# Kernel optimization log

Hardware: AMD Instinct MI355X
Metric: run time of the kernel (lower is better)

The kernel has to match this reference:

```python
import jax, jax.numpy as jnp
import numpy as np

B, T, DM, H = 2, 2048, 2048, 16
D = DM // H  # 128
STD = 0.02


def setup_inputs() -> dict:
    key = jax.random.key(0)
    ks = jax.random.split(key, 8)
    inner = H * D
    x = jax.random.normal(ks[0], (B, T, DM), jnp.float32)
    state = jnp.zeros((B, H, D, D), jnp.float32)
    Wq = jax.random.normal(ks[1], (inner, DM), jnp.float32) * STD
    Wk = jax.random.normal(ks[2], (inner, DM), jnp.float32) * STD
    Wv = jax.random.normal(ks[3], (inner, DM), jnp.float32) * STD
    Wa = jax.random.normal(ks[4], (inner, DM), jnp.float32) * STD
    ba = jnp.zeros((inner,), jnp.float32)
    Wb = jax.random.normal(ks[5], (H, DM), jnp.float32) * STD
    bb = jnp.zeros((H,), jnp.float32)
    Wg = jax.random.normal(ks[6], (inner, DM), jnp.float32) * STD
    bg = jnp.zeros((inner,), jnp.float32)
    Wo = jax.random.normal(ks[7], (DM, inner), jnp.float32) * STD
    return {"x": x, "state": state, "Wq": Wq, "Wk": Wk, "Wv": Wv,
            "Wa": Wa, "ba": ba, "Wb": Wb, "bb": bb, "Wg": Wg, "bg": bg, "Wo": Wo}


def _l2norm(t):
    # matches torch F.normalize(p=2, dim=-1, eps=1e-12)
    n = jnp.sqrt(jnp.sum(t * t, axis=-1, keepdims=True))
    return t / jnp.maximum(n, 1e-12)


def reference(x, state, Wq, Wk, Wv, Wa, ba, Wb, bb, Wg, bg, Wo):
    b, t, _ = x.shape
    q = _l2norm((x @ Wq.T).reshape(b, t, H, D))
    k = _l2norm((x @ Wk.T).reshape(b, t, H, D))
    v = (x @ Wv.T).reshape(b, t, H, D)
    alpha = jax.nn.sigmoid(x @ Wa.T + ba).reshape(b, t, H, D)
    beta = jax.nn.sigmoid(x @ Wb.T + bb)  # (B,T,H)

    def step(S, inp):
        q_t, k_t, v_t, a_t, b_t = inp  # (B,H,D) x4, (B,H)
        Sk = jnp.einsum('bhij,bhj->bhi', S, k_t)
        delta = v_t - Sk
        S = a_t[..., None] * S + (b_t[..., None] * delta)[..., None] * k_t[:, :, None, :]
        out_t = jnp.einsum('bhij,bhj->bhi', S, q_t)
        return S, out_t

    xs = tuple(jnp.moveaxis(a, 1, 0) for a in (q, k, v, alpha, beta))
    _, outs = jax.lax.scan(step, state, xs)  # outs: (T,B,H,D)
    out = jnp.moveaxis(outs, 0, 1)  # (B,T,H,D)
    g = jax.nn.sigmoid(x @ Wg.T + bg).reshape(b, t, H, D)
    out = (out * g).reshape(b, t, H * D) @ Wo.T
    return out
```

## Files before the change

kernel.cpp:

```cpp
#include <hip/hip_runtime.h>
#include <hip/hip_bf16.h>

typedef short short8 __attribute__((ext_vector_type(8)));
typedef float f32x4 __attribute__((ext_vector_type(4)));

#define DEV __device__ __forceinline__
#define AS1 __attribute__((address_space(1)))
#define AS3 __attribute__((address_space(3)))

DEV void async_load16(const void* g, void* l) {
    __builtin_amdgcn_global_load_lds((const AS1 unsigned int*)g, (AS3 unsigned int*)l, 16, 0, 0);
}

template <int CTRL>
DEV float dpp_add16(float v) {
    int t = __builtin_amdgcn_update_dpp(0, __float_as_int(v), CTRL, 0xf, 0xf, true);
    return v + __int_as_float(t);
}
DEV float row_sum16(float v) {
    v = dpp_add16<0x128>(v);
    v = dpp_add16<0x124>(v);
    v = dpp_add16<0x122>(v);
    v = dpp_add16<0x121>(v);
    return v;
}

__global__ __launch_bounds__(256) void cast_bf16_kernel(const float* __restrict__ in,
                                                        __hip_bfloat16* __restrict__ out, int n) {
    int i = (blockIdx.x * 256 + threadIdx.x) * 4;
    if (i < n) {
        float4 v = *(const float4*)&in[i];
        out[i + 0] = __float2bfloat16(v.x);
        out[i + 1] = __float2bfloat16(v.y);
        out[i + 2] = __float2bfloat16(v.z);
        out[i + 3] = __float2bfloat16(v.w);
    }
}

__global__ __launch_bounds__(256) void cast6_kernel(const float* __restrict__ s0, const float* __restrict__ s1,
                                                    const float* __restrict__ s2, const float* __restrict__ s3,
                                                    const float* __restrict__ s4, const float* __restrict__ s5,
                                                    __hip_bfloat16* __restrict__ dst) {
    const int sec = blockIdx.x >> 12;
    const int loc = blockIdx.x & 4095;
    const float* s = sec == 0 ? s0 : sec == 1 ? s1 : sec == 2 ? s2 : sec == 3 ? s3 : sec == 4 ? s4 : s5;
    const int i = (loc * 256 + threadIdx.x) * 4;
    float4 v = *(const float4*)&s[i];
    __hip_bfloat16* o = dst + (size_t)sec * 4194304 + i;
    o[0] = __float2bfloat16(v.x);
    o[1] = __float2bfloat16(v.y);
    o[2] = __float2bfloat16(v.z);
    o[3] = __float2bfloat16(v.w);
}

template <int EPI>
__global__ __launch_bounds__(512, 2) void gemm256_fused(
        const short* __restrict__ A, const short* __restrict__ Bm,
        float* __restrict__ C, const float* __restrict__ bias1,
        const float* __restrict__ bias2, int M, int N, int K) {
    __shared__ short lds_s[65536];

    const int tid  = threadIdx.x;
    const int lane = tid & 63;
    const int w    = tid >> 6;
    const int wave_m = w >> 2;
    const int wave_n = w & 3;
    const int fr  = lane & 15;
    const int fk2 = (lane >> 4) * 16;
    const int er  = (lane >> 4) * 4;
    const int ec  = lane & 15;

    const int nbx = M >> 8;
    const int wg  = blockIdx.x;
    const int nwg = gridDim.x;
    const int cpx = nwg >> 3;
    const int swz = (wg & 7) * cpx + (wg >> 3);
    const int m0 = (swz & (nbx - 1)) * 256;
    const int n0 = (swz / nbx) * 256;

    const int Kb = K * 2;

    f32x4 acc[8][4] = {};

#define AREG(d, kh) (((d) * 2 + (kh)) << 14)
#define BREG(d, kh) (65536 + (((d) * 2 + (kh)) << 14))

    const int sr0 = w * 32 + (lane >> 2);
    const int sr1 = sr0 + 16;
    const int kbl = (lane & 3) * 16;
    auto STAGE = [&](const short* mat, int rc0, int tkoff, int region) {
        const char* g0 = (const char*)mat + (size_t)(rc0 + sr0) * Kb + tkoff + (kbl ^ (((sr0 >> 1) & 3) << 4));
        const char* g1 = (const char*)mat + (size_t)(rc0 + sr1) * Kb + tkoff + (kbl ^ (((sr1 >> 1) & 3) << 4));
        async_load16(g0, &lds_s[(region + w * 2048) >> 1]);
        async_load16(g1, &lds_s[(region + w * 2048 + 1024) >> 1]);
    };
    auto RDA = [&](int region, int i) -> short8 {
        const int ra = wave_m * 128 + i * 16 + fr;
        return *(const short8*)&lds_s[(region + ra * 64 + (fk2 ^ (((ra >> 1) & 3) << 4))) >> 1];
    };
    auto RDB = [&](int region, int j) -> short8 {
        const int cl = wave_n * 64 + j * 16 + fr;
        return *(const short8*)&lds_s[(region + cl * 64 + (fk2 ^ (((cl >> 1) & 3) << 4))) >> 1];
    };

    STAGE(A,  m0, 0,   AREG(0, 0));  STAGE(A,  m0, 64,  AREG(0, 1));
    STAGE(Bm, n0, 0,   BREG(0, 0));  STAGE(Bm, n0, 64,  BREG(0, 1));
    STAGE(A,  m0, 128, AREG(1, 0));  STAGE(A,  m0, 192, AREG(1, 1));
    STAGE(Bm, n0, 128, BREG(1, 0));  STAGE(Bm, n0, 192, BREG(1, 1));
    asm volatile("s_waitcnt vmcnt(0)" ::: "memory");
    __builtin_amdgcn_s_barrier();
    __builtin_amdgcn_sched_barrier(0);

    short8 af[8], b0, b1;
    const int NT = K >> 6;

#define MFMA8(JA, JB)                                                            \
    __builtin_amdgcn_s_setprio(1);                                               \
    _Pragma("unroll") for (int i = 0; i < 8; i++)                                \
        acc[i][JA] = __builtin_amdgcn_mfma_f32_16x16x32_bf16(af[i], b0, acc[i][JA], 0, 0, 0); \
    _Pragma("unroll") for (int i = 0; i < 8; i++)                                \
        acc[i][JB] = __builtin_amdgcn_mfma_f32_16x16x32_bf16(af[i], b1, acc[i][JB], 0, 0, 0); \
    __builtin_amdgcn_s_setprio(0);

#define ENDPH()                                                                  \
    __builtin_amdgcn_s_barrier();                                                \
    __builtin_amdgcn_sched_barrier(0);

#define KTILE(D, T)                                                              \
    {                                                                            \
        _Pragma("unroll") for (int i = 0; i < 8; i++) af[i] = RDA(AREG(D, 0), i);\
        b0 = RDB(BREG(D, 0), 0); b1 = RDB(BREG(D, 0), 1);                        \
        STAGE(Bm, n0, ((T) + 1) * 128 + 64, BREG(D ^ 1, 1));                     \
        MFMA8(0, 1)                                                              \
        ENDPH()                                                                  \
        b0 = RDB(BREG(D, 0), 2); b1 = RDB(BREG(D, 0), 3);                        \
        STAGE(A, m0, ((T) + 2) * 128, AREG(D, 0));                               \
        MFMA8(2, 3)                                                              \
        ENDPH()                                                                  \
        _Pragma("unroll") for (int i = 0; i < 8; i++) af[i] = RDA(AREG(D, 1), i);\
        b0 = RDB(BREG(D, 1), 0); b1 = RDB(BREG(D, 1), 1);                        \
        STAGE(Bm, n0, ((T) + 2) * 128, BREG(D, 0));                              \
        MFMA8(0, 1)                                                              \
        ENDPH()                                                                  \
        b0 = RDB(BREG(D, 1), 2); b1 = RDB(BREG(D, 1), 3);                        \
        STAGE(A, m0, ((T) + 2) * 128 + 64, AREG(D, 1));                          \
        MFMA8(2, 3)                                                              \
        asm volatile("s_waitcnt vmcnt(6)" ::: "memory");                         \
        ENDPH()                                                                  \
    }

    for (int T = 0; T < NT; T += 2) {
        KTILE(0, T)
        KTILE(1, T + 1)
    }
#undef KTILE
#undef ENDPH
#undef MFMA8

    if constexpr (EPI == 2) {
        const bool isqk = (n0 < 4096);
        if (isqk) {
            __syncthreads();
            float* lsum = (float*)lds_s;
#pragma unroll
            for (int i = 0; i < 8; i++) {
                float p[4];
#pragma unroll
                for (int r = 0; r < 4; r++) {
                    float s = acc[i][0][r] * acc[i][0][r] + acc[i][1][r] * acc[i][1][r]
                            + acc[i][2][r] * acc[i][2][r] + acc[i][3][r] * acc[i][3][r];
                    p[r] = row_sum16(s);
                }
                if (ec == 0) {
                    const int R = wave_m * 128 + i * 16 + er;
                    lsum[wave_n * 256 + R + 0] = p[0];
                    lsum[wave_n * 256 + R + 1] = p[1];
                    lsum[wave_n * 256 + R + 2] = p[2];
                    lsum[wave_n * 256 + R + 3] = p[3];
                }
            }
            __syncthreads();
            const int h0 = (wave_n & 2);
#pragma unroll
            for (int i = 0; i < 8; i++)
#pragma unroll
                for (int r = 0; r < 4; r++) {
                    const int R = wave_m * 128 + i * 16 + er + r;
                    const float tot = lsum[h0 * 256 + R] + lsum[(h0 + 1) * 256 + R];
                    const float inv = 1.f / fmaxf(sqrtf(tot), 1e-12f);
#pragma unroll
                    for (int j = 0; j < 4; j++) acc[i][j][r] *= inv;
                }
        }
    }

    bool sig = false;
    const float* bp = nullptr;
    if constexpr (EPI == 2) {
        sig = (n0 >= 6144);
        if (sig) bp = (n0 >= 8192) ? (bias2 + (n0 - 8192)) : (bias1 + (n0 - 6144));
    }

#pragma unroll
    for (int i = 0; i < 8; i++) {
        const int gr = m0 + wave_m * 128 + i * 16 + er;
#pragma unroll
        for (int j = 0; j < 4; j++) {
            const int gc = n0 + wave_n * 64 + j * 16 + ec;
            float bia = 0.f;
            if constexpr (EPI == 2) { if (sig) bia = bp[wave_n * 64 + j * 16 + ec]; }
#pragma unroll
            for (int r = 0; r < 4; r++) {
                float v = acc[i][j][r];
                if constexpr (EPI == 2) { if (sig) v = 1.f / (1.f + __expf(-(v + bia))); }
                C[(size_t)(gr + r) * N + gc] = v;
            }
        }
    }
    asm volatile("s_waitcnt vmcnt(0)" ::: "memory");
}

__global__ __launch_bounds__(256) void beta_kernel(const float* __restrict__ x,
                                                   const float* __restrict__ Wb,
                                                   const float* __restrict__ bb,
                                                   float* __restrict__ beta) {
    __shared__ float xs[16 * 132];
    const int tid = threadIdx.x;
    const float* xr = &x[(size_t)blockIdx.x * 2048];
#pragma unroll
    for (int i = tid; i < 512; i += 256) {
        float4 v = ((const float4*)xr)[i];
        const int j = i * 4;
        *(float4*)&xs[(j >> 7) * 132 + (j & 127)] = v;
    }
    __syncthreads();
    const int n = tid >> 4, ks = tid & 15;
    const float* wv = &Wb[(size_t)n * 2048 + ks * 128];
    const float* xx = &xs[ks * 132];
    float s = 0.f;
#pragma unroll 8
    for (int j = 0; j < 128; j++) s += xx[j] * wv[j];
    s += __shfl_xor(s, 1); s += __shfl_xor(s, 2);
    s += __shfl_xor(s, 4); s += __shfl_xor(s, 8);
    if (ks == 0) beta[(size_t)blockIdx.x * 16 + n] = 1.f / (1.f + __expf(-(s + bb[n])));
}

__global__ __launch_bounds__(256)
__attribute__((amdgpu_waves_per_eu(1, 1)))
void recurrence_kernel(
        const float* __restrict__ S0, const float* __restrict__ qall,
        const float* __restrict__ bet, __hip_bfloat16* __restrict__ o) {
    __shared__ __hip_bfloat16 lout[4][64][4];

    const int bh  = blockIdx.x & 31;
    const int rb8 = blockIdx.x >> 5;
    const int b = bh >> 4, h = bh & 15;
    const int lane = threadIdx.x & 63;
    const int wave = threadIdx.x >> 6;
    const int r = lane >> 4;
    const int c = lane & 15;
    const int i0 = rb8 * 16 + wave * 4;
    const int i = i0 + r;

    f32x4 S40, S41;
    {
        const float* s0 = &S0[((size_t)(bh * 128 + i)) * 128 + c * 8];
        S40 = *(const f32x4*)s0;
        S41 = *(const f32x4*)(s0 + 4);
    }

    const unsigned SB = 10240 * 4;
    const float* rowb = qall + (size_t)(b * 2048) * 10240 + h * 128;
    const float* qbase = rowb;
    const float* kbase = rowb + 2048;
    const float* vbase = rowb + 4096;
    const float* abase = rowb + 6144;
    const float* gbase = rowb + 8192;
    const float* bbase = bet + (size_t)(b * 2048) * 16 + h;
    char* ob = (char*)(o + ((size_t)(b * 2048) * 16 + h) * 128 + i0);

    unsigned voff_kq = (unsigned)(c * 32);
    unsigned voff_i  = (unsigned)(i * 4);
    unsigned voff_b  = 0;

    f32x4 kA0, kA1, qA0, qA1; float vA, aA, gA, bA;
    f32x4 kB0, kB1, qB0, qB1; float vB, aB, gB, bB;
    f32x4 kC0, kC1, qC0, qC1; float vC, aC, gC, bC;
    f32x4 kD0, kD1, qD0, qD1; float vD, aD, gD, bD;

#define ISSUE(SET)                                                              \
    asm volatile("global_load_dwordx4 %0, %2, %3\n\t"                           \
                 "global_load_dwordx4 %1, %2, %3 offset:16"                     \
                 : "=v"(k##SET##0), "=v"(k##SET##1)                             \
                 : "v"(voff_kq), "s"(kbase));                                   \
    asm volatile("global_load_dwordx4 %0, %2, %3\n\t"                           \
                 "global_load_dwordx4 %1, %2, %3 offset:16"                     \
                 : "=v"(q##SET##0), "=v"(q##SET##1)                             \
                 : "v"(voff_kq), "s"(qbase));                                   \
    asm volatile("global_load_dword %0, %1, %2"                                 \
                 : "=v"(v##SET) : "v"(voff_i), "s"(vbase));                     \
    asm volatile("global_load_dword %0, %1, %2"                                 \
                 : "=v"(a##SET) : "v"(voff_i), "s"(abase));                     \
    asm volatile("global_load_dword %0, %1, %2"                                 \
                 : "=v"(g##SET) : "v"(voff_i), "s"(gbase));                     \
    asm volatile("global_load_dword %0, %1, %2"                                 \
                 : "=v"(b##SET) : "v"(voff_b), "s"(bbase));

#define ADV() { voff_kq += SB; voff_i += SB; voff_b += 64; }

    ISSUE(A); ADV();
    ISSUE(B); ADV();
    ISSUE(C); ADV();
    ISSUE(D); ADV();

#define BODY(SLOT, SET)                                                   \
    {                                                                     \
        asm volatile("s_waitcnt vmcnt(24)");                              \
        asm volatile("" : "+v"(k##SET##0), "+v"(k##SET##1),               \
                          "+v"(q##SET##0), "+v"(q##SET##1),               \
                          "+v"(v##SET), "+v"(a##SET),                     \
                          "+v"(g##SET), "+v"(b##SET));                    \
        f32x4 ps = S40 * k##SET##0;                                       \
        ps = S41 * k##SET##1 + ps;                                        \
        float p = row_sum16((ps[0] + ps[1]) + (ps[2] + ps[3]));           \
        const float coef = b##SET * (v##SET - p);                         \
        S40 = a##SET * S40 + coef * k##SET##0;                            \
        S41 = a##SET * S41 + coef * k##SET##1;                            \
        f32x4 os = S40 * q##SET##0;                                       \
        os = S41 * q##SET##1 + os;                                        \
        float ov = row_sum16((os[0] + os[1]) + (os[2] + os[3]));          \
        if (c == 0) lout[wave][(SLOT)][r] = __float2bfloat16(ov * g##SET);\
        ISSUE(SET);                                                       \
        ADV();                                                            \
    }

    for (int tb = 0; tb < 2048; tb += 64) {
        for (int tt = 0; tt < 64; tt += 4) {
            BODY(tt,     A);
            BODY(tt + 1, B);
            BODY(tt + 2, C);
            BODY(tt + 3, D);
        }
        uint2 pk = *(const uint2*)&lout[wave][lane][0];
        *(uint2*)(ob + (size_t)(tb + lane) * 4096) = pk;
    }
#undef BODY
#undef ADV
#undef ISSUE
}

extern "C" void kernel_launch(void* const* d_in, const int* in_sizes, int n_in,
                              void* d_out, int out_size, void* d_ws, size_t ws_size,
                              hipStream_t stream) {
    const float* x  = (const float*)d_in[0];
    const float* S0 = (const float*)d_in[1];
    const float* Wq = (const float*)d_in[2];
    const float* Wk = (const float*)d_in[3];
    const float* Wv = (const float*)d_in[4];
    const float* Wa = (const float*)d_in[5];
    const float* ba = (const float*)d_in[6];
    const float* Wb = (const float*)d_in[7];
    const float* bb = (const float*)d_in[8];
    const float* Wg = (const float*)d_in[9];
    const float* bg = (const float*)d_in[10];
    const float* Wo = (const float*)d_in[11];
    float* out = (float*)d_out;

    const int M = 4096, K = 2048;
    const int NF = 10240;
    const size_t SLACK = 16 * (size_t)NF * 4;

    size_t off = 0;
    auto alloc = [&](size_t bytes) {
        void* p = (char*)d_ws + off;
        off += (bytes + 255) & ~(size_t)255;
        return p;
    };
    short* x_bf  = (short*)alloc((size_t)M * K * 2);
    short* W_bf  = (short*)alloc((size_t)6 * K * K * 2);
    float* qall  = (float*)alloc((size_t)M * NF * 4 + SLACK);
    float* betab = (float*)alloc((size_t)M * 16 * 4 + 65536);

    cast_bf16_kernel<<<dim3(M * K / 1024), dim3(256), 0, stream>>>(x, (__hip_bfloat16*)x_bf, M * K);
    cast6_kernel<<<dim3(6 * 4096), dim3(256), 0, stream>>>(Wq, Wk, Wv, Wa, Wg, Wo, (__hip_bfloat16*)W_bf);

    gemm256_fused<2><<<dim3((M / 256) * (NF / 256)), dim3(512), 0, stream>>>(
        x_bf, W_bf, qall, ba, bg, M, NF, K);

    beta_kernel<<<dim3(M), dim3(256), 0, stream>>>(x, Wb, bb, betab);

    __hip_bfloat16* o_bf = (__hip_bfloat16*)x_bf;
    recurrence_kernel<<<dim3(256), dim3(256), 0, stream>>>(S0, qall, betab, o_bf);

    gemm256_fused<0><<<dim3((M / 256) * (K / 256)), dim3(512), 0, stream>>>(
        (const short*)o_bf, W_bf + (size_t)5 * K * K, out, nullptr, nullptr, M, K, K);
}
```

Baseline: 643.8 us.

## Process two state row-blocks per thread in recurrence, halving block count

Each thread in the recurrence kernel now holds two row slices of the state matrix (rows i and i+64), so the k and q vector loads are shared across two rows. The grid shrinks from 256 to 128 blocks, and the per-step load count goes from 8 to 11 with the wait threshold adjusted to match. This cuts redundant k/q loads and per-step overhead, and exposes two independent reduction chains per step for more ILP. The cost is more registers per thread and fewer blocks to spread across the GPU's compute units.

```diff
diff --git a/kernel.cpp b/kernel.cpp
--- a/kernel.cpp
+++ b/kernel.cpp
@@ -24,6 +24,7 @@
     v = dpp_add16<0x121>(v);
     return v;
 }
+DEV float hadd4(f32x4 v) { return (v[0] + v[1]) + (v[2] + v[3]); }
 
 __global__ __launch_bounds__(256) void cast_bf16_kernel(const float* __restrict__ in,
                                                         __hip_bfloat16* __restrict__ out, int n) {
@@ -250,23 +251,27 @@
 void recurrence_kernel(
         const float* __restrict__ S0, const float* __restrict__ qall,
         const float* __restrict__ bet, __hip_bfloat16* __restrict__ o) {
-    __shared__ __hip_bfloat16 lout[4][64][4];
-
-    const int bh  = blockIdx.x & 31;
-    const int rb8 = blockIdx.x >> 5;
+    __shared__ __hip_bfloat16 lout1[4][64][4];
+    __shared__ __hip_bfloat16 lout2[4][64][4];
+
+    const int bh = blockIdx.x & 31;
+    const int rb = blockIdx.x >> 5;
     const int b = bh >> 4, h = bh & 15;
     const int lane = threadIdx.x & 63;
     const int wave = threadIdx.x >> 6;
     const int r = lane >> 4;
     const int c = lane & 15;
-    const int i0 = rb8 * 16 + wave * 4;
+    const int i0 = rb * 16 + wave * 4;
     const int i = i0 + r;
 
-    f32x4 S40, S41;
+    f32x4 S10, S11, S20, S21;
     {
-        const float* s0 = &S0[((size_t)(bh * 128 + i)) * 128 + c * 8];
-        S40 = *(const f32x4*)s0;
-        S41 = *(const f32x4*)(s0 + 4);
+        const float* s1 = &S0[((size_t)(bh * 128 + i)) * 128 + c * 8];
+        S10 = *(const f32x4*)s1;
+        S11 = *(const f32x4*)(s1 + 4);
+        const float* s2 = s1 + (size_t)64 * 128;
+        S20 = *(const f32x4*)s2;
+        S21 = *(const f32x4*)(s2 + 4);
     }
 
     const unsigned SB = 10240 * 4;
@@ -277,16 +282,17 @@
     const float* abase = rowb + 6144;
     const float* gbase = rowb + 8192;
     const float* bbase = bet + (size_t)(b * 2048) * 16 + h;
-    char* ob = (char*)(o + ((size_t)(b * 2048) * 16 + h) * 128 + i0);
+    char* ob1 = (char*)(o + ((size_t)(b * 2048) * 16 + h) * 128 + i0);
+    char* ob2 = ob1 + 128;
 
     unsigned voff_kq = (unsigned)(c * 32);
     unsigned voff_i  = (unsigned)(i * 4);
     unsigned voff_b  = 0;
 
-    f32x4 kA0, kA1, qA0, qA1; float vA, aA, gA, bA;
-    f32x4 kB0, kB1, qB0, qB1; float vB, aB, gB, bB;
-    f32x4 kC0, kC1, qC0, qC1; float vC, aC, gC, bC;
-    f32x4 kD0, kD1, qD0, qD1; float vD, aD, gD, bD;
+    f32x4 kA0, kA1, qA0, qA1; float vA, aA, gA, bA, v2A, a2A, g2A;
+    f32x4 kB0, kB1, qB0, qB1; float vB, aB, gB, bB, v2B, a2B, g2B;
+    f32x4 kC0, kC1, qC0, qC1; float vC, aC, gC, bC, v2C, a2C, g2C;
+    f32x4 kD0, kD1, qD0, qD1; float vD, aD, gD, bD, v2D, a2D, g2D;
 
 #define ISSUE(SET)                                                              \
     asm volatile("global_load_dwordx4 %0, %2, %3\n\t"                           \
@@ -304,7 +310,13 @@
     asm volatile("global_load_dword %0, %1, %2"                                 \
                  : "=v"(g##SET) : "v"(voff_i), "s"(gbase));                     \
     asm volatile("global_load_dword %0, %1, %2"                                 \
-                 : "=v"(b##SET) : "v"(voff_b), "s"(bbase));
+                 : "=v"(b##SET) : "v"(voff_b), "s"(bbase));                     \
+    asm volatile("global_load_dword %0, %1, %2 offset:256"                      \
+                 : "=v"(v2##SET) : "v"(voff_i), "s"(vbase));                    \
+    asm volatile("global_load_dword %0, %1, %2 offset:256"                      \
+                 : "=v"(a2##SET) : "v"(voff_i), "s"(abase));                    \
+    asm volatile("global_load_dword %0, %1, %2 offset:256"                      \
+                 : "=v"(g2##SET) : "v"(voff_i), "s"(gbase));
 
 #define ADV() { voff_kq += SB; voff_i += SB; voff_b += 64; }
 
@@ -313,25 +325,38 @@
     ISSUE(C); ADV();
     ISSUE(D); ADV();
 
-#define BODY(SLOT, SET)                                                   \
-    {                                                                     \
-        asm volatile("s_waitcnt vmcnt(24)");                              \
-        asm volatile("" : "+v"(k##SET##0), "+v"(k##SET##1),               \
-                          "+v"(q##SET##0), "+v"(q##SET##1),               \
-                          "+v"(v##SET), "+v"(a##SET),                     \
-                          "+v"(g##SET), "+v"(b##SET));                    \
-        f32x4 ps = S40 * k##SET##0;                                       \
-        ps = S41 * k##SET##1 + ps;                                        \
-        float p = row_sum16((ps[0] + ps[1]) + (ps[2] + ps[3]));           \
-        const float coef = b##SET * (v##SET - p);                         \
-        S40 = a##SET * S40 + coef * k##SET##0;                            \
-        S41 = a##SET * S41 + coef * k##SET##1;                            \
-        f32x4 os = S40 * q##SET##0;                                       \
-        os = S41 * q##SET##1 + os;                                        \
-        float ov = row_sum16((os[0] + os[1]) + (os[2] + os[3]));          \
-        if (c == 0) lout[wave][(SLOT)][r] = __float2bfloat16(ov * g##SET);\
-        ISSUE(SET);                                                       \
-        ADV();                                                            \
+#define BODY(SLOT, SET)                                                       \
+    {                                                                         \
+        asm volatile("s_waitcnt vmcnt(22)");                                  \
+        asm volatile("" : "+v"(k##SET##0), "+v"(k##SET##1),                   \
+                          "+v"(q##SET##0), "+v"(q##SET##1),                   \
+                          "+v"(v##SET), "+v"(a##SET),                         \
+                          "+v"(g##SET), "+v"(b##SET));                        \
+        asm volatile("" : "+v"(v2##SET), "+v"(a2##SET), "+v"(g2##SET));       \
+        f32x4 p1v = S10 * k##SET##0;                                          \
+        p1v = S11 * k##SET##1 + p1v;                                          \
+        f32x4 p2v = S20 * k##SET##0;                                          \
+        p2v = S21 * k##SET##1 + p2v;                                          \
+        float p1 = row_sum16(hadd4(p1v));                                     \
+        float p2 = row_sum16(hadd4(p2v));                                     \
+        const float coef1 = b##SET * (v##SET - p1);                           \
+        const float coef2 = b##SET * (v2##SET - p2);                          \
+        S10 = a##SET * S10 + coef1 * k##SET##0;                               \
+        S11 = a##SET * S11 + coef1 * k##SET##1;                               \
+        S20 = a2##SET * S20 + coef2 * k##SET##0;                              \
+        S21 = a2##SET * S21 + coef2 * k##SET##1;                              \
+        f32x4 o1v = S10 * q##SET##0;                                          \
+        o1v = S11 * q##SET##1 + o1v;                                          \
+        f32x4 o2v = S20 * q##SET##0;                                          \
+        o2v = S21 * q##SET##1 + o2v;                                          \
+        float ov1 = row_sum16(hadd4(o1v));                                    \
+        float ov2 = row_sum16(hadd4(o2v));                                    \
+        if (c == 0) {                                                         \
+            lout1[wave][(SLOT)][r] = __float2bfloat16(ov1 * g##SET);          \
+            lout2[wave][(SLOT)][r] = __float2bfloat16(ov2 * g2##SET);         \
+        }                                                                     \
+        ISSUE(SET);                                                           \
+        ADV();                                                                \
     }
 
     for (int tb = 0; tb < 2048; tb += 64) {
@@ -341,8 +366,10 @@
             BODY(tt + 2, C);
             BODY(tt + 3, D);
         }
-        uint2 pk = *(const uint2*)&lout[wave][lane][0];
-        *(uint2*)(ob + (size_t)(tb + lane) * 4096) = pk;
+        uint2 pk1 = *(const uint2*)&lout1[wave][lane][0];
+        *(uint2*)(ob1 + (size_t)(tb + lane) * 4096) = pk1;
+        uint2 pk2 = *(const uint2*)&lout2[wave][lane][0];
+        *(uint2*)(ob2 + (size_t)(tb + lane) * 4096) = pk2;
     }
 #undef BODY
 #undef ADV
@@ -390,7 +417,7 @@
     beta_kernel<<<dim3(M), dim3(256), 0, stream>>>(x, Wb, bb, betab);
 
     __hip_bfloat16* o_bf = (__hip_bfloat16*)x_bf;
-    recurrence_kernel<<<dim3(256), dim3(256), 0, stream>>>(S0, qall, betab, o_bf);
+    recurrence_kernel<<<dim3(128), dim3(256), 0, stream>>>(S0, qall, betab, o_bf);
 
     gemm256_fused<0><<<dim3((M / 256) * (K / 256)), dim3(512), 0, stream>>>(
         (const short*)o_bf, W_bf + (size_t)5 * K * K, out, nullptr, nullptr, M, K, K);
```

Result: slower. 801.4 us (+24.5%).
